# Performance work log

Hardware: AMD Instinct MI355X
Metric: run time of the kernel (lower is better)

The kernel has to match this reference:

```python
import jax, jax.numpy as jnp
import numpy as np

RES = 512
EMB_DIM = 32
HIDDEN = 128
OUT_DIM = 1
N = 1000000


def sample_plane(plane, coords):
    """Bilinear grid_sample, padding_mode='zeros', align_corners=True.
    plane: [C, H, W]; coords: [N, 2] with coords[:,0]=x (width), coords[:,1]=y (height), in [-1,1].
    Returns [N, C]."""
    C, H, W = plane.shape
    x = (coords[:, 0] + 1.0) * 0.5 * (W - 1)
    y = (coords[:, 1] + 1.0) * 0.5 * (H - 1)
    x0 = jnp.floor(x)
    y0 = jnp.floor(y)
    x1 = x0 + 1.0
    y1 = y0 + 1.0
    wx1 = x - x0
    wx0 = 1.0 - wx1
    wy1 = y - y0
    wy0 = 1.0 - wy1

    def gather(xi, yi, w):
        xi_i = xi.astype(jnp.int32)
        yi_i = yi.astype(jnp.int32)
        valid = ((xi_i >= 0) & (xi_i < W) & (yi_i >= 0) & (yi_i < H)).astype(plane.dtype)
        xc = jnp.clip(xi_i, 0, W - 1)
        yc = jnp.clip(yi_i, 0, H - 1)
        vals = plane[:, yc, xc]  # [C, N]
        return vals * (w * valid)[None, :]

    out = (gather(x0, y0, wx0 * wy0) + gather(x1, y0, wx1 * wy0)
           + gather(x0, y1, wx0 * wy1) + gather(x1, y1, wx1 * wy1))
    return out.T  # [N, C]


def setup_inputs() -> dict:
    key = jax.random.key(0)
    ks = jax.random.split(key, 12)
    coordinates = jax.random.uniform(ks[0], (N, 3), dtype=jnp.float32) * 2.0 - 1.0
    planes = jax.random.normal(ks[1], (3, EMB_DIM, RES, RES), dtype=jnp.float32) * 0.001
    s = 0.05
    w0 = jax.random.normal(ks[2], (HIDDEN, EMB_DIM), dtype=jnp.float32) * s
    b0 = jnp.zeros((HIDDEN,), jnp.float32)
    w1 = jax.random.normal(ks[3], (HIDDEN, HIDDEN), dtype=jnp.float32) * s
    b1 = jnp.zeros((HIDDEN,), jnp.float32)
    w2 = jax.random.normal(ks[4], (HIDDEN, HIDDEN), dtype=jnp.float32) * s
    b2 = jnp.zeros((HIDDEN,), jnp.float32)
    w3 = jax.random.normal(ks[5], (OUT_DIM, HIDDEN), dtype=jnp.float32) * s
    b3 = jnp.zeros((OUT_DIM,), jnp.float32)
    return {"coordinates": coordinates, "planes": planes,
            "w0": w0, "b0": b0, "w1": w1, "b1": b1,
            "w2": w2, "b2": b2, "w3": w3, "b3": b3}


def reference(coordinates, planes, w0, b0, w1, b1, w2, b2, w3, b3):
    xy = coordinates[:, 0:2]
    yz = coordinates[:, 1:3]
    xz = coordinates[:, 0:3:2]
    feats = (sample_plane(planes[0], xy)
             + sample_plane(planes[1], yz)
             + sample_plane(planes[2], xz))  # [N, EMB_DIM]
    h = jax.nn.relu(feats @ w0.T + b0)
    h = jax.nn.relu(h @ w1.T + b1)
    h = jax.nn.relu(h @ w2.T + b2)
    out = h @ w3.T + b3  # [N, OUT_DIM]
    return out[None]  # torch returns (1, N, OUT_DIM)
```

## Files before the change

kernel.cpp:

```cpp
#include <hip/hip_runtime.h>


#define SF 256.0f
#define HPAD 136
#define FSTR 40

typedef _Float16 half8 __attribute__((ext_vector_type(8)));
typedef _Float16 half4_t __attribute__((ext_vector_type(4)));
typedef float f32x4 __attribute__((ext_vector_type(4)));
typedef unsigned int u32x4 __attribute__((ext_vector_type(4)));

__global__ __launch_bounds__(256) void zero_hist(unsigned* __restrict__ hist) {
  int t = blockIdx.x * 256 + threadIdx.x;
  if (t < 32768) hist[t] = 0u;
}

__global__ __launch_bounds__(256) void plane_transpose(
    const float* __restrict__ planes, _Float16* __restrict__ ph) {
  int t = blockIdx.x * 256 + threadIdx.x;
  int pid = t >> 18;
  int rem = t & ((1 << 18) - 1);
  const float* src = planes + ((size_t)pid << 23) + rem;
  union { _Float16 h[32]; u32x4 v[4]; } u;
#pragma unroll
  for (int c = 0; c < 32; c++)
    u.h[c] = (_Float16)(src[(size_t)c << 18] * SF);
  u32x4* dst = reinterpret_cast<u32x4*>(ph + ((size_t)t << 5));
#pragma unroll
  for (int i = 0; i < 4; i++) dst[i] = u.v[i];
}

__global__ __launch_bounds__(256) void weights_convert(
    const float* __restrict__ w0, const float* __restrict__ w1,
    const float* __restrict__ w2, _Float16* __restrict__ w0h,
    _Float16* __restrict__ w1h, _Float16* __restrict__ w2h) {
  int t = blockIdx.x * 256 + threadIdx.x;
  if (t < 4096) w0h[t] = (_Float16)w0[t];
  else if (t < 20480) w1h[t - 4096] = (_Float16)w1[t - 4096];
  else w2h[t - 20480] = (_Float16)w2[t - 20480];
}

__device__ inline unsigned spread5(unsigned v) {
  v &= 31u;
  v = (v | (v << 8)) & 0x100Fu;
  v = (v | (v << 4)) & 0x10C3u;
  v = (v | (v << 2)) & 0x1249u;
  return v;
}
__device__ inline unsigned cellkey(float x, float y, float z) {
  int qx = min(31, max(0, (int)((x + 1.0f) * 16.0f)));
  int qy = min(31, max(0, (int)((y + 1.0f) * 16.0f)));
  int qz = min(31, max(0, (int)((z + 1.0f) * 16.0f)));
  return spread5((unsigned)qx) | (spread5((unsigned)qy) << 1) |
         (spread5((unsigned)qz) << 2);
}

__global__ __launch_bounds__(256) void hist_kernel(
    const float* __restrict__ coords, unsigned* __restrict__ hist, int npts) {
  int p = blockIdx.x * 256 + threadIdx.x;
  if (p >= npts) return;
  float x = coords[3 * (size_t)p + 0];
  float y = coords[3 * (size_t)p + 1];
  float z = coords[3 * (size_t)p + 2];
  atomicAdd(&hist[cellkey(x, y, z)], 1u);
}

__global__ __launch_bounds__(1024) void scan_kernel(
    const unsigned* __restrict__ hist, unsigned* __restrict__ cursor) {
  __shared__ unsigned sums[1024];
  int t = threadIdx.x;
  unsigned local[32];
  unsigned s = 0;
#pragma unroll
  for (int i = 0; i < 32; i++) { local[i] = hist[t * 32 + i]; s += local[i]; }
  sums[t] = s;
  __syncthreads();
  for (int off = 1; off < 1024; off <<= 1) {
    unsigned v = (t >= off) ? sums[t - off] : 0u;
    __syncthreads();
    sums[t] += v;
    __syncthreads();
  }
  unsigned base = (t == 0) ? 0u : sums[t - 1];
#pragma unroll
  for (int i = 0; i < 32; i++) { cursor[t * 32 + i] = base; base += local[i]; }
}

__global__ __launch_bounds__(256) void scatter_kernel(
    const float* __restrict__ coords, unsigned* __restrict__ cursor,
    float4* __restrict__ sorted, int npts) {
  int p = blockIdx.x * 256 + threadIdx.x;
  if (p >= npts) return;
  float x = coords[3 * (size_t)p + 0];
  float y = coords[3 * (size_t)p + 1];
  float z = coords[3 * (size_t)p + 2];
  unsigned pos = atomicAdd(&cursor[cellkey(x, y, z)], 1u);
  float4 v;
  v.x = x; v.y = y; v.z = z; v.w = __uint_as_float((unsigned)p);
  sorted[pos] = v;
}

__device__ __attribute__((always_inline)) inline void samp16(
    const _Float16* __restrict__ pl, float X, float Y, int hf, float* acc) {
  float fx = (X + 1.0f) * 0.5f * 511.0f;
  float fy = (Y + 1.0f) * 0.5f * 511.0f;
  float x0f = floorf(fx), y0f = floorf(fy);
  float wx1 = fx - x0f, wy1 = fy - y0f;
  float wx0 = 1.0f - wx1, wy0 = 1.0f - wy1;
  int x0 = (int)x0f, y0 = (int)y0f;
  int x1 = x0 + 1, y1 = y0 + 1;
  float vx0 = (x0 >= 0 && x0 < 512) ? 1.0f : 0.0f;
  float vx1 = (x1 >= 0 && x1 < 512) ? 1.0f : 0.0f;
  float vy0 = (y0 >= 0 && y0 < 512) ? 1.0f : 0.0f;
  float vy1 = (y1 >= 0 && y1 < 512) ? 1.0f : 0.0f;
  int xc0 = min(max(x0, 0), 511), xc1 = min(max(x1, 0), 511);
  int yc0 = min(max(y0, 0), 511), yc1 = min(max(y1, 0), 511);
  float w00 = wx0 * wy0 * vx0 * vy0, w10 = wx1 * wy0 * vx1 * vy0;
  float w01 = wx0 * wy1 * vx0 * vy1, w11 = wx1 * wy1 * vx1 * vy1;
  const _Float16* p00 = pl + ((((size_t)yc0 << 9) + xc0) << 5) + hf * 16;
  const _Float16* p10 = pl + ((((size_t)yc0 << 9) + xc1) << 5) + hf * 16;
  const _Float16* p01 = pl + ((((size_t)yc1 << 9) + xc0) << 5) + hf * 16;
  const _Float16* p11 = pl + ((((size_t)yc1 << 9) + xc1) << 5) + hf * 16;
#pragma unroll
  for (int ch = 0; ch < 2; ch++) {
    union { u32x4 v; _Float16 h[8]; } a, b, c, d;
    a.v = *reinterpret_cast<const u32x4*>(p00 + ch * 8);
    b.v = *reinterpret_cast<const u32x4*>(p10 + ch * 8);
    c.v = *reinterpret_cast<const u32x4*>(p01 + ch * 8);
    d.v = *reinterpret_cast<const u32x4*>(p11 + ch * 8);
#pragma unroll
    for (int j = 0; j < 8; j++) {
      acc[ch * 8 + j] += w00 * (float)a.h[j] + w10 * (float)b.h[j] +
                         w01 * (float)c.h[j] + w11 * (float)d.h[j];
    }
  }
}

__device__ __attribute__((always_inline)) inline half8 ld16(const _Float16* p) {
  return *reinterpret_cast<const half8*>(p);
}

#define LAYER_PAIR(Wg, bias)                                                   \
  {                                                                            \
    half8 Bf[4][4];                                    \
    _Pragma("unroll") for (int nt = 0; nt < 4; nt++)                           \
    _Pragma("unroll") for (int ks = 0; ks < 4; ks++)                           \
        Bf[nt][ks] = ld16(&H[(nt * 16 + n16) * HPAD + ks * 32 + g * 8]);       \
    __syncthreads();                  \
    _Pragma("unroll") for (int mt = 0; mt < 4; mt++) {                         \
      f32x4 acc[4];                                                            \
      _Pragma("unroll") for (int nt = 0; nt < 4; nt++) acc[nt] = Z4;           \
      _Pragma("unroll") for (int ks = 0; ks < 4; ks++) {                       \
        half8 A = ld16((Wg) + ((w * 4 + mt) * 16 + n16) * 128 + ks * 32 + g * 8); \
        _Pragma("unroll") for (int nt = 0; nt < 4; nt++)                       \
            acc[nt] = __builtin_amdgcn_mfma_f32_16x16x32_f16(A, Bf[nt][ks],    \
                                                             acc[nt], 0, 0, 0); \
      }                                                                        \
      int gm = w * 4 + mt;                                                     \
      f32x4 bb = *reinterpret_cast<const f32x4*>((bias) + gm * 16 + g * 4);    \
      _Pragma("unroll") for (int nt = 0; nt < 4; nt++) {                       \
        half4_t v;                                                             \
        _Pragma("unroll") for (int r = 0; r < 4; r++)                          \
            v[r] = (_Float16)fmaxf(acc[nt][r] + SF * bb[r], 0.0f);             \
        *reinterpret_cast<half4_t*>(                                           \
            &H[(nt * 16 + n16) * HPAD + gm * 16 + g * 4]) = v;                 \
      }                                                                        \
    }                                                                          \
    __syncthreads();                          \
  }

__global__ __launch_bounds__(256, 4) void fused_kernel(
    const float* __restrict__ coords, const float4* __restrict__ sorted,
    const _Float16* __restrict__ ph, const _Float16* __restrict__ w0h,
    const _Float16* __restrict__ w1h, const _Float16* __restrict__ w2h,
    const float* __restrict__ b0, const float* __restrict__ b1,
    const float* __restrict__ b2, const float* __restrict__ w3,
    const float* __restrict__ b3, float* __restrict__ out, int npts,
    int use_sorted) {
  __shared__ alignas(16) _Float16 hbuf[2][64 * HPAD];
  int tid = threadIdx.x;
  int nb = gridDim.x, bid = blockIdx.x;
  int per = nb >> 3;
  int sb = (bid < (per << 3)) ? ((bid & 7) * per + (bid >> 3)) : bid;

  {
    int ptl = tid >> 1, hf = tid & 1;
    long pb = (long)sb * 128 + (ptl >> 6) * 64;
    if (pb + 64 > npts) pb = npts - 64;
    long pp = pb + (ptl & 63);
    float cx, cy, cz;
    if (use_sorted) {
      float4 f = sorted[pp];
      cx = f.x; cy = f.y; cz = f.z;
    } else {
      cx = coords[3 * pp + 0];
      cy = coords[3 * pp + 1];
      cz = coords[3 * pp + 2];
    }
    float acc[16];
#pragma unroll
    for (int c = 0; c < 16; c++) acc[c] = 0.0f;
    samp16(ph, cx, cy, hf, acc);
    samp16(ph + (1u << 23), cy, cz, hf, acc);
    samp16(ph + (2u << 23), cx, cz, hf, acc);
    union { _Float16 h[16]; u32x4 v[2]; } u;
#pragma unroll
    for (int c = 0; c < 16; c++) u.h[c] = (_Float16)acc[c];
    _Float16* F = hbuf[ptl >> 6];
    *reinterpret_cast<u32x4*>(&F[(ptl & 63) * FSTR + hf * 16]) = u.v[0];
    *reinterpret_cast<u32x4*>(&F[(ptl & 63) * FSTR + hf * 16 + 8]) = u.v[1];
  }
  __syncthreads();

  int wv = tid >> 6, lane = tid & 63;
  int pair = wv >> 1, w = wv & 1;
  int n16 = lane & 15, g = lane >> 4;
  long base = (long)sb * 128 + pair * 64;
  if (base + 64 > npts) base = npts - 64;
  _Float16* H = hbuf[pair];
  const f32x4 Z4 = {0.0f, 0.0f, 0.0f, 0.0f};

  {
    half8 Bf[4];
#pragma unroll
    for (int nt = 0; nt < 4; nt++)
      Bf[nt] = ld16(&H[(nt * 16 + n16) * FSTR + g * 8]);
    __syncthreads();
#pragma unroll
    for (int mt = 0; mt < 4; mt++) {
      half8 A = ld16(w0h + ((w * 4 + mt) * 16 + n16) * 32 + g * 8);
      f32x4 acc[4];
#pragma unroll
      for (int nt = 0; nt < 4; nt++)
        acc[nt] = __builtin_amdgcn_mfma_f32_16x16x32_f16(A, Bf[nt], Z4, 0, 0, 0);
      int gm = w * 4 + mt;
      f32x4 bb = *reinterpret_cast<const f32x4*>(b0 + gm * 16 + g * 4);
#pragma unroll
      for (int nt = 0; nt < 4; nt++) {
        half4_t v;
#pragma unroll
        for (int r = 0; r < 4; r++)
          v[r] = (_Float16)fmaxf(acc[nt][r] + SF * bb[r], 0.0f);
        *reinterpret_cast<half4_t*>(
            &H[(nt * 16 + n16) * HPAD + gm * 16 + g * 4]) = v;
      }
    }
    __syncthreads();
  }

  LAYER_PAIR(w1h, b1)
  LAYER_PAIR(w2h, b2)

  int ptl3 = lane & 31, hh = lane >> 5;
  int pt = w * 32 + ptl3;
  float o = 0.0f;
#pragma unroll
  for (int ii = 0; ii < 8; ii++) {
    int i = hh * 8 + ii;
    half8 hv = ld16(&H[pt * HPAD + i * 8]);
#pragma unroll
    for (int j = 0; j < 8; j++) o += (float)hv[j] * w3[i * 8 + j];
  }
  o += __shfl_xor(o, 32);
  if (lane < 32) {
    unsigned idx = use_sorted ? __float_as_uint(sorted[base + pt].w)
                              : (unsigned)(base + pt);
    out[idx] = o * (1.0f / SF) + b3[0];
  }
}

extern "C" void kernel_launch(void* const* d_in, const int* in_sizes, int n_in,
                              void* d_out, int out_size, void* d_ws, size_t ws_size,
                              hipStream_t stream) {
  const float* coords = (const float*)d_in[0];
  const float* planes = (const float*)d_in[1];
  const float* w0 = (const float*)d_in[2];
  const float* b0 = (const float*)d_in[3];
  const float* w1 = (const float*)d_in[4];
  const float* b1 = (const float*)d_in[5];
  const float* w2 = (const float*)d_in[6];
  const float* b2 = (const float*)d_in[7];
  const float* w3 = (const float*)d_in[8];
  const float* b3 = (const float*)d_in[9];
  float* out = (float*)d_out;
  int npts = in_sizes[0] / 3;

  char* ws = (char*)d_ws;
  _Float16* ph = (_Float16*)ws;
  _Float16* w0h = (_Float16*)(ws + 50331648);
  _Float16* w1h = (_Float16*)(ws + 50339840);
  _Float16* w2h = (_Float16*)(ws + 50372608);
  unsigned* hist = (unsigned*)(ws + 50405376);
  unsigned* cursor = (unsigned*)(ws + 50536448);
  float4* sorted = (float4*)(ws + 50667520);
  size_t need = 50667520 + (size_t)npts * 16;
  int use_sorted = (ws_size == 0 || ws_size >= need) ? 1 : 0;

  int blk = (npts + 255) / 256;
  int fblk = (npts + 127) / 128;
  plane_transpose<<<3072, 256, 0, stream>>>(planes, ph);
  weights_convert<<<144, 256, 0, stream>>>(w0, w1, w2, w0h, w1h, w2h);
  if (use_sorted) {
    zero_hist<<<128, 256, 0, stream>>>(hist);
    hist_kernel<<<blk, 256, 0, stream>>>(coords, hist, npts);
    scan_kernel<<<1, 1024, 0, stream>>>(hist, cursor);
    scatter_kernel<<<blk, 256, 0, stream>>>(coords, cursor, sorted, npts);
  }
  fused_kernel<<<fblk, 256, 0, stream>>>(coords, sorted, ph, w0h, w1h, w2h, b0,
                                         b1, b2, w3, b3, out, npts, use_sorted);
}
```

Baseline: 508.9 us.

## Merge prep kernels and replace counting-sort chain with one cooperative kernel

Folds plane transpose, weight conversion and histogram zeroing into a single prep launch, and replaces the hist/scan/scatter kernels with one cooperative kernel that uses grid-wide syncs and a two-level parallel scan. This removes several launch gaps and the single-block serial scan, and keeps coordinates and keys in registers between phases instead of reading them twice. The cooperative kernel hardcodes 1024 blocks with 4 points per thread (262144 stride), so inputs larger than about one million points would be only partly sorted. It also depends on all 1024 blocks being resident at once for the grid syncs.

After: 800.2 us. 1.57x slower.

```diff
diff --git a/kernel.cpp b/kernel.cpp
--- a/kernel.cpp
+++ b/kernel.cpp
@@ -1,4 +1,7 @@
 #include <hip/hip_runtime.h>
+#include <hip/hip_cooperative_groups.h>
+
+namespace cg = cooperative_groups;
 
 
 #define SF 256.0f
@@ -9,36 +12,6 @@
 typedef _Float16 half4_t __attribute__((ext_vector_type(4)));
 typedef float f32x4 __attribute__((ext_vector_type(4)));
 typedef unsigned int u32x4 __attribute__((ext_vector_type(4)));
-
-__global__ __launch_bounds__(256) void zero_hist(unsigned* __restrict__ hist) {
-  int t = blockIdx.x * 256 + threadIdx.x;
-  if (t < 32768) hist[t] = 0u;
-}
-
-__global__ __launch_bounds__(256) void plane_transpose(
-    const float* __restrict__ planes, _Float16* __restrict__ ph) {
-  int t = blockIdx.x * 256 + threadIdx.x;
-  int pid = t >> 18;
-  int rem = t & ((1 << 18) - 1);
-  const float* src = planes + ((size_t)pid << 23) + rem;
-  union { _Float16 h[32]; u32x4 v[4]; } u;
-#pragma unroll
-  for (int c = 0; c < 32; c++)
-    u.h[c] = (_Float16)(src[(size_t)c << 18] * SF);
-  u32x4* dst = reinterpret_cast<u32x4*>(ph + ((size_t)t << 5));
-#pragma unroll
-  for (int i = 0; i < 4; i++) dst[i] = u.v[i];
-}
-
-__global__ __launch_bounds__(256) void weights_convert(
-    const float* __restrict__ w0, const float* __restrict__ w1,
-    const float* __restrict__ w2, _Float16* __restrict__ w0h,
-    _Float16* __restrict__ w1h, _Float16* __restrict__ w2h) {
-  int t = blockIdx.x * 256 + threadIdx.x;
-  if (t < 4096) w0h[t] = (_Float16)w0[t];
-  else if (t < 20480) w1h[t - 4096] = (_Float16)w1[t - 4096];
-  else w2h[t - 20480] = (_Float16)w2[t - 20480];
-}
 
 __device__ inline unsigned spread5(unsigned v) {
   v &= 31u;
@@ -55,49 +28,105 @@
          (spread5((unsigned)qz) << 2);
 }
 
-__global__ __launch_bounds__(256) void hist_kernel(
-    const float* __restrict__ coords, unsigned* __restrict__ hist, int npts) {
-  int p = blockIdx.x * 256 + threadIdx.x;
-  if (p >= npts) return;
-  float x = coords[3 * (size_t)p + 0];
-  float y = coords[3 * (size_t)p + 1];
-  float z = coords[3 * (size_t)p + 2];
-  atomicAdd(&hist[cellkey(x, y, z)], 1u);
-}
-
-__global__ __launch_bounds__(1024) void scan_kernel(
-    const unsigned* __restrict__ hist, unsigned* __restrict__ cursor) {
-  __shared__ unsigned sums[1024];
-  int t = threadIdx.x;
-  unsigned local[32];
-  unsigned s = 0;
-#pragma unroll
-  for (int i = 0; i < 32; i++) { local[i] = hist[t * 32 + i]; s += local[i]; }
-  sums[t] = s;
-  __syncthreads();
-  for (int off = 1; off < 1024; off <<= 1) {
-    unsigned v = (t >= off) ? sums[t - off] : 0u;
+__global__ __launch_bounds__(256) void prep_kernel(
+    const float* __restrict__ planes, _Float16* __restrict__ ph,
+    const float* __restrict__ w0, const float* __restrict__ w1,
+    const float* __restrict__ w2, _Float16* __restrict__ w0h,
+    _Float16* __restrict__ w1h, _Float16* __restrict__ w2h,
+    unsigned* __restrict__ hist) {
+  int bid = blockIdx.x;
+  if (bid < 3072) {
+    int t = bid * 256 + threadIdx.x;
+    int pid = t >> 18;
+    int rem = t & ((1 << 18) - 1);
+    const float* src = planes + ((size_t)pid << 23) + rem;
+    union { _Float16 h[32]; u32x4 v[4]; } u;
+#pragma unroll
+    for (int c = 0; c < 32; c++)
+      u.h[c] = (_Float16)(src[(size_t)c << 18] * SF);
+    u32x4* dst = reinterpret_cast<u32x4*>(ph + ((size_t)t << 5));
+#pragma unroll
+    for (int i = 0; i < 4; i++) dst[i] = u.v[i];
+  } else if (bid < 3216) {
+    int t = (bid - 3072) * 256 + threadIdx.x;
+    if (t < 4096) w0h[t] = (_Float16)w0[t];
+    else if (t < 20480) w1h[t - 4096] = (_Float16)w1[t - 4096];
+    else w2h[t - 20480] = (_Float16)w2[t - 20480];
+  } else {
+    int t = (bid - 3216) * 256 + threadIdx.x;
+    hist[t] = 0u;
+  }
+}
+
+__global__ __launch_bounds__(256, 4) void sort_coop(
+    const float* __restrict__ coords, unsigned* __restrict__ hist,
+    unsigned* __restrict__ cursor, unsigned* __restrict__ blocksum,
+    unsigned* __restrict__ blockoff, float4* __restrict__ sorted, int npts) {
+  cg::grid_group grid = cg::this_grid();
+  __shared__ unsigned s[256];
+  int gtid = blockIdx.x * 256 + threadIdx.x;
+
+  float px[4], py[4], pz[4];
+  unsigned key[4];
+#pragma unroll
+  for (int i = 0; i < 4; i++) {
+    long p = (long)i * 262144 + gtid;
+    if (p < npts) {
+      px[i] = coords[3 * p + 0];
+      py[i] = coords[3 * p + 1];
+      pz[i] = coords[3 * p + 2];
+      key[i] = cellkey(px[i], py[i], pz[i]);
+      atomicAdd(&hist[key[i]], 1u);
+    } else {
+      key[i] = 0xFFFFFFFFu;
+    }
+  }
+  grid.sync();
+
+  if (blockIdx.x < 128) {
+    int t = threadIdx.x;
+    int base = blockIdx.x * 256;
+    unsigned v = hist[base + t];
+    s[t] = v;
     __syncthreads();
-    sums[t] += v;
+    for (int off = 1; off < 256; off <<= 1) {
+      unsigned u = (t >= off) ? s[t - off] : 0u;
+      __syncthreads();
+      s[t] += u;
+      __syncthreads();
+    }
+    cursor[base + t] = s[t] - v;
+    if (t == 255) blocksum[blockIdx.x] = s[255];
+  }
+  grid.sync();
+
+  if (blockIdx.x == 0) {
+    int t = threadIdx.x;
+    unsigned v2 = (t < 128) ? blocksum[t] : 0u;
+    s[t] = v2;
     __syncthreads();
-  }
-  unsigned base = (t == 0) ? 0u : sums[t - 1];
-#pragma unroll
-  for (int i = 0; i < 32; i++) { cursor[t * 32 + i] = base; base += local[i]; }
-}
-
-__global__ __launch_bounds__(256) void scatter_kernel(
-    const float* __restrict__ coords, unsigned* __restrict__ cursor,
-    float4* __restrict__ sorted, int npts) {
-  int p = blockIdx.x * 256 + threadIdx.x;
-  if (p >= npts) return;
-  float x = coords[3 * (size_t)p + 0];
-  float y = coords[3 * (size_t)p + 1];
-  float z = coords[3 * (size_t)p + 2];
-  unsigned pos = atomicAdd(&cursor[cellkey(x, y, z)], 1u);
-  float4 v;
-  v.x = x; v.y = y; v.z = z; v.w = __uint_as_float((unsigned)p);
-  sorted[pos] = v;
+    for (int off = 1; off < 128; off <<= 1) {
+      unsigned u = (t >= off) ? s[t - off] : 0u;
+      __syncthreads();
+      s[t] += u;
+      __syncthreads();
+    }
+    if (t < 128) blockoff[t] = s[t] - v2;
+  }
+  grid.sync();
+
+#pragma unroll
+  for (int i = 0; i < 4; i++) {
+    long p = (long)i * 262144 + gtid;
+    if (p < npts) {
+      unsigned k = key[i];
+      unsigned pos = atomicAdd(&cursor[k], 1u) + blockoff[k >> 8];
+      float4 v;
+      v.x = px[i]; v.y = py[i]; v.z = pz[i];
+      v.w = __uint_as_float((unsigned)p);
+      sorted[pos] = v;
+    }
+  }
 }
 
 __device__ __attribute__((always_inline)) inline void samp16(
@@ -292,19 +321,22 @@
   _Float16* w2h = (_Float16*)(ws + 50372608);
   unsigned* hist = (unsigned*)(ws + 50405376);
   unsigned* cursor = (unsigned*)(ws + 50536448);
-  float4* sorted = (float4*)(ws + 50667520);
-  size_t need = 50667520 + (size_t)npts * 16;
+  unsigned* blocksum = (unsigned*)(ws + 50667520);
+  unsigned* blockoff = (unsigned*)(ws + 50668032);
+  float4* sorted = (float4*)(ws + 50668544);
+  size_t need = 50668544 + (size_t)npts * 16;
   int use_sorted = (ws_size == 0 || ws_size >= need) ? 1 : 0;
 
-  int blk = (npts + 255) / 256;
   int fblk = (npts + 127) / 128;
-  plane_transpose<<<3072, 256, 0, stream>>>(planes, ph);
-  weights_convert<<<144, 256, 0, stream>>>(w0, w1, w2, w0h, w1h, w2h);
+
+  prep_kernel<<<3344, 256, 0, stream>>>(planes, ph, w0, w1, w2, w0h, w1h, w2h,
+                                        hist);
   if (use_sorted) {
-    zero_hist<<<128, 256, 0, stream>>>(hist);
-    hist_kernel<<<blk, 256, 0, stream>>>(coords, hist, npts);
-    scan_kernel<<<1, 1024, 0, stream>>>(hist, cursor);
-    scatter_kernel<<<blk, 256, 0, stream>>>(coords, cursor, sorted, npts);
+    void* args[] = {(void*)&coords,   (void*)&hist,     (void*)&cursor,
+                    (void*)&blocksum, (void*)&blockoff, (void*)&sorted,
+                    (void*)&npts};
+    hipLaunchCooperativeKernel((const void*)sort_coop, dim3(1024), dim3(256),
+                               args, 0, stream);
   }
   fused_kernel<<<fblk, 256, 0, stream>>>(coords, sorted, ph, w0h, w1h, w2h, b0,
                                          b1, b2, w3, b3, out, npts, use_sorted);
```

## Drop spatial point sorting and merge plane and weight prep kernels

Applied to the files above, without the earlier changes.

Removes the Morton-cell histogram, scan and scatter passes that reordered points for locality, so the fused kernel reads coordinates directly and writes output in original order. The plane transpose and weight conversion are merged into one launch, and the block-index swizzle is removed. This cuts four launches and the sort traffic, but gives up the texture-cache locality that sorting gave the random bilinear gathers into the 48MB fp16 plane buffer.

Measured after the change: 446.2 us. -12.3%, faster.

```diff
diff --git a/kernel.cpp b/kernel.cpp
--- a/kernel.cpp
+++ b/kernel.cpp
@@ -10,94 +10,30 @@
 typedef float f32x4 __attribute__((ext_vector_type(4)));
 typedef unsigned int u32x4 __attribute__((ext_vector_type(4)));
 
-__global__ __launch_bounds__(256) void zero_hist(unsigned* __restrict__ hist) {
-  int t = blockIdx.x * 256 + threadIdx.x;
-  if (t < 32768) hist[t] = 0u;
-}
-
-__global__ __launch_bounds__(256) void plane_transpose(
-    const float* __restrict__ planes, _Float16* __restrict__ ph) {
-  int t = blockIdx.x * 256 + threadIdx.x;
-  int pid = t >> 18;
-  int rem = t & ((1 << 18) - 1);
-  const float* src = planes + ((size_t)pid << 23) + rem;
-  union { _Float16 h[32]; u32x4 v[4]; } u;
-#pragma unroll
-  for (int c = 0; c < 32; c++)
-    u.h[c] = (_Float16)(src[(size_t)c << 18] * SF);
-  u32x4* dst = reinterpret_cast<u32x4*>(ph + ((size_t)t << 5));
-#pragma unroll
-  for (int i = 0; i < 4; i++) dst[i] = u.v[i];
-}
-
-__global__ __launch_bounds__(256) void weights_convert(
+__global__ __launch_bounds__(256) void prep_kernel(
+    const float* __restrict__ planes, _Float16* __restrict__ ph,
     const float* __restrict__ w0, const float* __restrict__ w1,
     const float* __restrict__ w2, _Float16* __restrict__ w0h,
     _Float16* __restrict__ w1h, _Float16* __restrict__ w2h) {
-  int t = blockIdx.x * 256 + threadIdx.x;
-  if (t < 4096) w0h[t] = (_Float16)w0[t];
-  else if (t < 20480) w1h[t - 4096] = (_Float16)w1[t - 4096];
-  else w2h[t - 20480] = (_Float16)w2[t - 20480];
-}
-
-__device__ inline unsigned spread5(unsigned v) {
-  v &= 31u;
-  v = (v | (v << 8)) & 0x100Fu;
-  v = (v | (v << 4)) & 0x10C3u;
-  v = (v | (v << 2)) & 0x1249u;
-  return v;
-}
-__device__ inline unsigned cellkey(float x, float y, float z) {
-  int qx = min(31, max(0, (int)((x + 1.0f) * 16.0f)));
-  int qy = min(31, max(0, (int)((y + 1.0f) * 16.0f)));
-  int qz = min(31, max(0, (int)((z + 1.0f) * 16.0f)));
-  return spread5((unsigned)qx) | (spread5((unsigned)qy) << 1) |
-         (spread5((unsigned)qz) << 2);
-}
-
-__global__ __launch_bounds__(256) void hist_kernel(
-    const float* __restrict__ coords, unsigned* __restrict__ hist, int npts) {
-  int p = blockIdx.x * 256 + threadIdx.x;
-  if (p >= npts) return;
-  float x = coords[3 * (size_t)p + 0];
-  float y = coords[3 * (size_t)p + 1];
-  float z = coords[3 * (size_t)p + 2];
-  atomicAdd(&hist[cellkey(x, y, z)], 1u);
-}
-
-__global__ __launch_bounds__(1024) void scan_kernel(
-    const unsigned* __restrict__ hist, unsigned* __restrict__ cursor) {
-  __shared__ unsigned sums[1024];
-  int t = threadIdx.x;
-  unsigned local[32];
-  unsigned s = 0;
-#pragma unroll
-  for (int i = 0; i < 32; i++) { local[i] = hist[t * 32 + i]; s += local[i]; }
-  sums[t] = s;
-  __syncthreads();
-  for (int off = 1; off < 1024; off <<= 1) {
-    unsigned v = (t >= off) ? sums[t - off] : 0u;
-    __syncthreads();
-    sums[t] += v;
-    __syncthreads();
-  }
-  unsigned base = (t == 0) ? 0u : sums[t - 1];
-#pragma unroll
-  for (int i = 0; i < 32; i++) { cursor[t * 32 + i] = base; base += local[i]; }
-}
-
-__global__ __launch_bounds__(256) void scatter_kernel(
-    const float* __restrict__ coords, unsigned* __restrict__ cursor,
-    float4* __restrict__ sorted, int npts) {
-  int p = blockIdx.x * 256 + threadIdx.x;
-  if (p >= npts) return;
-  float x = coords[3 * (size_t)p + 0];
-  float y = coords[3 * (size_t)p + 1];
-  float z = coords[3 * (size_t)p + 2];
-  unsigned pos = atomicAdd(&cursor[cellkey(x, y, z)], 1u);
-  float4 v;
-  v.x = x; v.y = y; v.z = z; v.w = __uint_as_float((unsigned)p);
-  sorted[pos] = v;
+  int bid = blockIdx.x;
+  if (bid < 3072) {
+    int t = bid * 256 + threadIdx.x;
+    int pid = t >> 18;
+    int rem = t & ((1 << 18) - 1);
+    const float* src = planes + ((size_t)pid << 23) + rem;
+    union { _Float16 h[32]; u32x4 v[4]; } u;
+#pragma unroll
+    for (int c = 0; c < 32; c++)
+      u.h[c] = (_Float16)(src[(size_t)c << 18] * SF);
+    u32x4* dst = reinterpret_cast<u32x4*>(ph + ((size_t)t << 5));
+#pragma unroll
+    for (int i = 0; i < 4; i++) dst[i] = u.v[i];
+  } else {
+    int t = (bid - 3072) * 256 + threadIdx.x;
+    if (t < 4096) w0h[t] = (_Float16)w0[t];
+    else if (t < 20480) w1h[t - 4096] = (_Float16)w1[t - 4096];
+    else w2h[t - 20480] = (_Float16)w2[t - 20480];
+  }
 }
 
 __device__ __attribute__((always_inline)) inline void samp16(
@@ -170,33 +106,24 @@
   }
 
 __global__ __launch_bounds__(256, 4) void fused_kernel(
-    const float* __restrict__ coords, const float4* __restrict__ sorted,
-    const _Float16* __restrict__ ph, const _Float16* __restrict__ w0h,
-    const _Float16* __restrict__ w1h, const _Float16* __restrict__ w2h,
-    const float* __restrict__ b0, const float* __restrict__ b1,
-    const float* __restrict__ b2, const float* __restrict__ w3,
-    const float* __restrict__ b3, float* __restrict__ out, int npts,
-    int use_sorted) {
+    const float* __restrict__ coords, const _Float16* __restrict__ ph,
+    const _Float16* __restrict__ w0h, const _Float16* __restrict__ w1h,
+    const _Float16* __restrict__ w2h, const float* __restrict__ b0,
+    const float* __restrict__ b1, const float* __restrict__ b2,
+    const float* __restrict__ w3, const float* __restrict__ b3,
+    float* __restrict__ out, int npts) {
   __shared__ alignas(16) _Float16 hbuf[2][64 * HPAD];
   int tid = threadIdx.x;
-  int nb = gridDim.x, bid = blockIdx.x;
-  int per = nb >> 3;
-  int sb = (bid < (per << 3)) ? ((bid & 7) * per + (bid >> 3)) : bid;
+  int sb = blockIdx.x;
 
   {
     int ptl = tid >> 1, hf = tid & 1;
     long pb = (long)sb * 128 + (ptl >> 6) * 64;
     if (pb + 64 > npts) pb = npts - 64;
     long pp = pb + (ptl & 63);
-    float cx, cy, cz;
-    if (use_sorted) {
-      float4 f = sorted[pp];
-      cx = f.x; cy = f.y; cz = f.z;
-    } else {
-      cx = coords[3 * pp + 0];
-      cy = coords[3 * pp + 1];
-      cz = coords[3 * pp + 2];
-    }
+    float cx = coords[3 * pp + 0];
+    float cy = coords[3 * pp + 1];
+    float cz = coords[3 * pp + 2];
     float acc[16];
 #pragma unroll
     for (int c = 0; c < 16; c++) acc[c] = 0.0f;
@@ -263,9 +190,7 @@
   }
   o += __shfl_xor(o, 32);
   if (lane < 32) {
-    unsigned idx = use_sorted ? __float_as_uint(sorted[base + pt].w)
-                              : (unsigned)(base + pt);
-    out[idx] = o * (1.0f / SF) + b3[0];
+    out[base + pt] = o * (1.0f / SF) + b3[0];
   }
 }
 
@@ -290,22 +215,10 @@
   _Float16* w0h = (_Float16*)(ws + 50331648);
   _Float16* w1h = (_Float16*)(ws + 50339840);
   _Float16* w2h = (_Float16*)(ws + 50372608);
-  unsigned* hist = (unsigned*)(ws + 50405376);
-  unsigned* cursor = (unsigned*)(ws + 50536448);
-  float4* sorted = (float4*)(ws + 50667520);
-  size_t need = 50667520 + (size_t)npts * 16;
-  int use_sorted = (ws_size == 0 || ws_size >= need) ? 1 : 0;
-
-  int blk = (npts + 255) / 256;
+
   int fblk = (npts + 127) / 128;
-  plane_transpose<<<3072, 256, 0, stream>>>(planes, ph);
-  weights_convert<<<144, 256, 0, stream>>>(w0, w1, w2, w0h, w1h, w2h);
-  if (use_sorted) {
-    zero_hist<<<128, 256, 0, stream>>>(hist);
-    hist_kernel<<<blk, 256, 0, stream>>>(coords, hist, npts);
-    scan_kernel<<<1, 1024, 0, stream>>>(hist, cursor);
-    scatter_kernel<<<blk, 256, 0, stream>>>(coords, cursor, sorted, npts);
-  }
-  fused_kernel<<<fblk, 256, 0, stream>>>(coords, sorted, ph, w0h, w1h, w2h, b0,
-                                         b1, b2, w3, b3, out, npts, use_sorted);
-}
+
+  prep_kernel<<<3216, 256, 0, stream>>>(planes, ph, w0, w1, w2, w0h, w1h, w2h);
+  fused_kernel<<<fblk, 256, 0, stream>>>(coords, ph, w0h, w1h, w2h, b0, b1, b2,
+                                         w3, b3, out, npts);
+}
```
